# Kernel optimization log

Measured on AMD Instinct MI355X. Metric: run time of the kernel, lower is better.

Reference implementation:

```python
import jax, jax.numpy as jnp
import numpy as np

C = 128      # in = out channels
H = 4        # heads
HD = C // H  # head dim
N_DRUG, N_DIS, E = 50000, 20000, 250000
EA_DIM = 8


def _seg_softmax(logits, seg, n):
    # torch_geometric.utils.softmax: per-destination-node softmax over incident edges
    m = jax.ops.segment_max(logits, seg, num_segments=n)          # [n,H]
    ex = jnp.exp(logits - m[seg])
    s = jax.ops.segment_sum(ex, seg, num_segments=n)
    return ex / (s[seg] + 1e-16)


def _edge_conv(src_x, dst_x, si, di, Ws, bs, Wd, bd, attn, gate, n_dst):
    msg_src = src_x[si] @ Ws + bs           # [E,C] gather + linear
    msg_dst = dst_x[di] @ Wd + bd
    msg = msg_src + msg_dst
    if gate is not None:
        msg = msg * gate
    e = msg.shape[0]
    mh = msg.reshape(e, H, HD)
    sh = msg_src.reshape(e, H, HD)
    dh = msg_dst.reshape(e, H, HD)
    logits = (sh * dh).sum(-1) / jnp.sqrt(jnp.float32(HD)) + (mh * attn).sum(-1)  # [E,H]
    w = _seg_softmax(logits, di, n_dst)
    out = (mh * w[..., None]).reshape(e, C)
    return jax.ops.segment_sum(out, di, num_segments=n_dst)      # [n_dst,C]


def setup_inputs() -> dict:
    key = jax.random.key(0)
    ks = jax.random.split(key, 24)
    s = 1.0 / np.sqrt(C)
    d = {
        'x_drug': jax.random.normal(ks[0], (N_DRUG, C), jnp.float32),
        'x_disease': jax.random.normal(ks[1], (N_DIS, C), jnp.float32),
        'ea_treats': jax.random.normal(ks[2], (E, EA_DIM), jnp.float32),
        'si_t': jax.random.randint(ks[3], (E,), 0, N_DRUG),
        'di_t': jax.random.randint(ks[4], (E,), 0, N_DIS),
        'si_r': jax.random.randint(ks[5], (E,), 0, N_DIS),
        'di_r': jax.random.randint(ks[6], (E,), 0, N_DRUG),
        'Ws_t': jax.random.normal(ks[7], (C, C), jnp.float32) * s,
        'bs_t': jnp.zeros((C,), jnp.float32),
        'Wd_t': jax.random.normal(ks[8], (C, C), jnp.float32) * s,
        'bd_t': jnp.zeros((C,), jnp.float32),
        'attn_t': jax.random.normal(ks[9], (1, H, HD), jnp.float32) * 0.1,
        'Wg1': jax.random.normal(ks[10], (EA_DIM, C), jnp.float32) * (1.0 / np.sqrt(EA_DIM)),
        'bg1': jnp.zeros((C,), jnp.float32),
        'Wg2': jax.random.normal(ks[11], (C, C), jnp.float32) * s,
        'bg2': jnp.zeros((C,), jnp.float32),
        'Ws_r': jax.random.normal(ks[12], (C, C), jnp.float32) * s,
        'bs_r': jnp.zeros((C,), jnp.float32),
        'Wd_r': jax.random.normal(ks[13], (C, C), jnp.float32) * s,
        'bd_r': jnp.zeros((C,), jnp.float32),
        'attn_r': jax.random.normal(ks[14], (1, H, HD), jnp.float32) * 0.1,
        'Wo_drug': jax.random.normal(ks[15], (C, C), jnp.float32) * s,
        'bo_drug': jnp.zeros((C,), jnp.float32),
        'Wo_dis': jax.random.normal(ks[16], (C, C), jnp.float32) * s,
        'bo_dis': jnp.zeros((C,), jnp.float32),
    }
    return d


def reference(x_drug, x_disease, ea_treats, si_t, di_t, si_r, di_r,
              Ws_t, bs_t, Wd_t, bd_t, attn_t, Wg1, bg1, Wg2, bg2,
              Ws_r, bs_r, Wd_r, bd_r, attn_r,
              Wo_drug, bo_drug, Wo_dis, bo_dis):
    # edge gate for (drug, treats, disease): continuous edge attrs -> Linear-GELU-Linear-Sigmoid
    gate = jax.nn.sigmoid(jax.nn.gelu(ea_treats @ Wg1 + bg1, approximate=False) @ Wg2 + bg2)
    aggr_dis = _edge_conv(x_drug, x_disease, si_t, di_t, Ws_t, bs_t, Wd_t, bd_t, attn_t, gate, N_DIS)
    aggr_drug = _edge_conv(x_disease, x_drug, si_r, di_r, Ws_r, bs_r, Wd_r, bd_r, attn_r, None, N_DRUG)
    # single message per node type -> mean is identity; then per-node-type lin_out
    out_drug = aggr_drug @ Wo_drug + bo_drug
    out_dis = aggr_dis @ Wo_dis + bo_dis
    return out_drug, out_dis
```

## Files before the change

kernel.cpp:

```cpp
#include <hip/hip_runtime.h>
#include <hip/hip_bf16.h>
#include <math.h>

#define N_DRUG 50000
#define N_DIS  20000
#define NE     250000
#define NE_PAD 250048

#define NB0 79
#define NBT 275

typedef __bf16 bf16x8 __attribute__((ext_vector_type(8)));
typedef __bf16 bf16x4 __attribute__((ext_vector_type(4)));
typedef __bf16 bf16x2 __attribute__((ext_vector_type(2)));
typedef float  f32x4  __attribute__((ext_vector_type(4)));
typedef float  f32x2  __attribute__((ext_vector_type(2)));

__device__ __forceinline__ bf16x8 bz8() {
  bf16x8 v;
  #pragma unroll
  for (int j = 0; j < 8; ++j) v[j] = (__bf16)0.f;
  return v;
}

__device__ __forceinline__ float gelu_fast(float x) {
  float ax = fabsf(x);
  float t = fmaf(ax, 0.019527f, 3.43654e-4f);
  t = fmaf(ax, t, 0.1151945f);
  t = fmaf(ax, t, 0.1968564f);
  float p = fmaf(ax, t, 1.0f);
  float p2 = p * p;
  float p4 = p2 * p2;
  float r = __builtin_amdgcn_rcpf(p4);
  float sel = (x >= 0.f) ? (2.0f - r) : r;
  return 0.5f * x * sel;
}

__device__ __forceinline__ float sigmoid_fast(float v) {
  return __builtin_amdgcn_rcpf(1.0f + __expf(-v));
}

template <int N>
__device__ __forceinline__ float dpp_ror(float v) {
  int r = __builtin_amdgcn_update_dpp(0, __builtin_bit_cast(int, v),
                                      0x120 | N, 0xF, 0xF, false);
  return __builtin_bit_cast(float, r);
}

struct Seg {
  const void* A[4];
  const float* W[4];
  const float* bias[4];
  void* out[4];
  int M[4];
  int bstart[5];
};

template <int AIN_BF16, int OUT_BF16>
__global__ __launch_bounds__(256)
void gemm_seg(Seg d)
{
  __shared__ __bf16 Wt[128][136];

  const int b = blockIdx.x;
  const int sidx = (b >= d.bstart[3]) ? 3 : (b >= d.bstart[2]) ? 2
                 : (b >= d.bstart[1]) ? 1 : 0;
  const int nb = d.bstart[sidx + 1] - d.bstart[sidx];
  const int lb = b - d.bstart[sidx];
  const float* W = d.W[sidx];
  const float* bias = d.bias[sidx];
  const int M = d.M[sidx];
  const int ntiles = (M + 63) >> 6;
  const int tid = threadIdx.x;
  const int wv = tid >> 6, lane = tid & 63;
  const int m16 = lane & 15, quad = lane >> 4;

  for (int idx = tid; idx < 16384; idx += 256) {
    int k = idx >> 7, n = idx & 127;
    Wt[n][k] = (__bf16)W[idx];
  }
  __syncthreads();

  float bv[8];
  #pragma unroll
  for (int ct = 0; ct < 8; ++ct) bv[ct] = bias[ct * 16 + m16];

  auto load_afr = [&](int t, bf16x8* afr) {
    const int arow = (t << 6) + wv * 16 + m16;
    const bool ok = (t < ntiles) && (arow < M);
    if (AIN_BF16) {
      const __bf16* ap = (const __bf16*)d.A[sidx] + (long)arow * 128 + quad * 8;
      #pragma unroll
      for (int kt = 0; kt < 4; ++kt)
        afr[kt] = ok ? *(const bf16x8*)(ap + kt * 32) : bz8();
    } else {
      const float* ap = (const float*)d.A[sidx] + (long)arow * 128 + quad * 8;
      #pragma unroll
      for (int kt = 0; kt < 4; ++kt) {
        bf16x8 v = bz8();
        if (ok) {
          f32x4 lo = *(const f32x4*)(ap + kt * 32);
          f32x4 hi = *(const f32x4*)(ap + kt * 32 + 4);
          #pragma unroll
          for (int j = 0; j < 4; ++j) { v[j] = (__bf16)lo[j]; v[4 + j] = (__bf16)hi[j]; }
        }
        afr[kt] = v;
      }
    }
  };

  bf16x8 afr[4];
  if (lb < ntiles) load_afr(lb, afr);

  for (int t = lb; t < ntiles; t += nb) {
    bf16x8 nafr[4];
    load_afr(t + nb, nafr);

    f32x4 acc[8];
    #pragma unroll
    for (int ct = 0; ct < 8; ++ct) acc[ct] = (f32x4){0.f, 0.f, 0.f, 0.f};
    #pragma unroll
    for (int kt = 0; kt < 4; ++kt) {
      #pragma unroll
      for (int ct = 0; ct < 8; ++ct) {
        bf16x8 bfr = *(const bf16x8*)&Wt[ct * 16 + m16][kt * 32 + quad * 8];
        acc[ct] = __builtin_amdgcn_mfma_f32_16x16x32_bf16(afr[kt], bfr, acc[ct], 0, 0, 0);
      }
    }

    const int rb = (t << 6) + wv * 16 + quad * 4;
    #pragma unroll
    for (int ct = 0; ct < 8; ++ct) {
      const int col = ct * 16 + m16;
      #pragma unroll
      for (int rg = 0; rg < 4; ++rg) {
        int gr = rb + rg;
        if (gr < M) {
          float v = acc[ct][rg] + bv[ct];
          if (OUT_BF16) ((__bf16*)d.out[sidx])[(long)gr * 128 + col] = (__bf16)v;
          else          ((float*)d.out[sidx])[(long)gr * 128 + col] = v;
        }
      }
    }
    #pragma unroll
    for (int kt = 0; kt < 4; ++kt) afr[kt] = nafr[kt];
  }
}

__global__ __launch_bounds__(256)
void gate_kernel(const float* __restrict__ EA, const float* __restrict__ W2,
                 const float* __restrict__ Wg1, const float* __restrict__ bg1,
                 const float* __restrict__ bg2, const int* __restrict__ sorted_t,
                 __bf16* __restrict__ out)
{
  __shared__ __bf16 Wt[128][132];
  __shared__ __bf16 H[64][132];
  const int tid = threadIdx.x;
  const int wv = tid >> 6, lane = tid & 63;
  const int m16 = lane & 15, quad = lane >> 4;

  for (int idx = tid; idx < 16384; idx += 256) {
    int k = idx >> 7, n = idx & 127;
    Wt[n][k] = (__bf16)W2[idx];
  }
  __syncthreads();

  bf16x8 b1[8];
  #pragma unroll
  for (int ct = 0; ct < 8; ++ct) {
    bf16x8 v = bz8();
    if (quad == 0) {
      #pragma unroll
      for (int j = 0; j < 8; ++j) v[j] = (__bf16)Wg1[j * 128 + ct * 16 + m16];
    }
    b1[ct] = v;
  }
  float b1v[8], b2v[8];
  #pragma unroll
  for (int ct = 0; ct < 8; ++ct) {
    b1v[ct] = bg1[ct * 16 + m16];
    b2v[ct] = bg2[ct * 16 + m16];
  }

  const int ntiles = (NE + 63) >> 6;
  const int hr = wv * 16 + quad * 4;
  const int ar = wv * 16 + m16;

  for (int t = blockIdx.x; t < ntiles; t += gridDim.x) {
    const int p = (t << 6) + wv * 16 + m16;

    bf16x8 a1 = bz8();
    if (quad == 0 && p < NE) {
      int e = sorted_t[p];
      f32x4 e0 = *(const f32x4*)(EA + (long)e * 8);
      f32x4 e1 = *(const f32x4*)(EA + (long)e * 8 + 4);
      #pragma unroll
      for (int j = 0; j < 4; ++j) { a1[j] = (__bf16)e0[j]; a1[4 + j] = (__bf16)e1[j]; }
    }
    f32x4 h[8];
    #pragma unroll
    for (int ct = 0; ct < 8; ++ct)
      h[ct] = __builtin_amdgcn_mfma_f32_16x16x32_bf16(a1, b1[ct], (f32x4){0.f,0.f,0.f,0.f}, 0, 0, 0);

    #pragma unroll
    for (int ct = 0; ct < 8; ++ct) {
      const int col = ct * 16 + m16;
      #pragma unroll
      for (int rg = 0; rg < 4; ++rg)
        H[hr + rg][col] = (__bf16)gelu_fast(h[ct][rg] + b1v[ct]);
    }
    asm volatile("s_waitcnt lgkmcnt(0)" ::: "memory");

    bf16x8 afr[4];
    #pragma unroll
    for (int kt = 0; kt < 4; ++kt)
      afr[kt] = *(const bf16x8*)&H[ar][kt * 32 + quad * 8];
    asm volatile("" ::: "memory");

    f32x4 acc[8];
    #pragma unroll
    for (int ct = 0; ct < 8; ++ct) acc[ct] = (f32x4){0.f, 0.f, 0.f, 0.f};
    #pragma unroll
    for (int kt = 0; kt < 4; ++kt) {
      #pragma unroll
      for (int ct = 0; ct < 8; ++ct) {
        bf16x8 bfr = *(const bf16x8*)&Wt[ct * 16 + m16][kt * 32 + quad * 8];
        acc[ct] = __builtin_amdgcn_mfma_f32_16x16x32_bf16(afr[kt], bfr, acc[ct], 0, 0, 0);
      }
    }

    const long rowbase = (long)(t << 6) + hr;
    #pragma unroll
    for (int ct = 0; ct < 8; ++ct) {
      const int col = ct * 16 + m16;
      #pragma unroll
      for (int rg = 0; rg < 4; ++rg)
        out[(rowbase + rg) * 128 + col] = (__bf16)sigmoid_fast(acc[ct][rg] + b2v[ct]);
    }
  }
}

__global__ __launch_bounds__(256)
void histo2(const int* __restrict__ di_t, const int* __restrict__ di_r,
            int* __restrict__ cnt_dis, int* __restrict__ cnt_drug, int half) {
  int b = blockIdx.x;
  if (b < half) {
    int i = b * 256 + threadIdx.x;
    if (i < NE) atomicAdd(&cnt_dis[di_t[i]], 1);
  } else {
    int i = (b - half) * 256 + threadIdx.x;
    if (i < NE) atomicAdd(&cnt_drug[di_r[i]], 1);
  }
}

__global__ __launch_bounds__(256)
void scatter2(const int* __restrict__ di_t, const int* __restrict__ di_r,
              const int* __restrict__ si_t, const int* __restrict__ si_r,
              int* __restrict__ cur_dis, int* __restrict__ cur_drug,
              int* __restrict__ sorted_t, int* __restrict__ ssrc_t,
              int* __restrict__ ssrc_r, int half) {
  int b = blockIdx.x;
  if (b < half) {
    int i = b * 256 + threadIdx.x;
    if (i < NE) {
      int p = atomicAdd(&cur_dis[di_t[i]], 1);
      sorted_t[p] = i;
      ssrc_t[p] = si_t[i];
    }
  } else {
    int i = (b - half) * 256 + threadIdx.x;
    if (i < NE) {
      int p = atomicAdd(&cur_drug[di_r[i]], 1);
      ssrc_r[p] = si_r[i];
    }
  }
}

__device__ __forceinline__ void seg_geom(int b, int& base, int& n, int& lb) {
  if (b < NB0) { base = 0;     n = 20000; lb = b; }
  else         { base = 20000; n = 50000; lb = b - NB0; }
}

__global__ __launch_bounds__(256)
void scan_partial(const int* __restrict__ cnt, int* __restrict__ bsum) {
  __shared__ int sh[256];
  int b = blockIdx.x, t = threadIdx.x;
  int base, n, lb; seg_geom(b, base, n, lb);
  int i = lb * 256 + t;
  sh[t] = (i < n) ? cnt[base + i] : 0;
  __syncthreads();
  for (int d = 1; d < 256; d <<= 1) {
    int vv = (t >= d) ? sh[t - d] : 0;
    __syncthreads();
    sh[t] += vv;
    __syncthreads();
  }
  if (t == 255) bsum[b] = sh[255];
}

__global__ __launch_bounds__(256)
void scan_final2(const int* __restrict__ cnt, const int* __restrict__ bsum,
                 int* __restrict__ offs, int* __restrict__ cursor) {
  __shared__ int v[512];
  __shared__ int f[512];
  __shared__ int sh[256];
  const int b = blockIdx.x, t = threadIdx.x;

  for (int i = t; i < 512; i += 256) {
    v[i] = (i < NBT) ? bsum[i] : 0;
    f[i] = (i == 0 || i == NB0 || i >= NBT) ? 1 : 0;
  }
  __syncthreads();
  for (int d = 1; d < 512; d <<= 1) {
    const int i0 = t, i1 = t + 256;
    int vv0 = 0, ff0 = 1, vv1 = 0, ff1 = 1;
    if (i0 >= d) { vv0 = v[i0 - d]; ff0 = f[i0 - d]; }
    if (i1 >= d) { vv1 = v[i1 - d]; ff1 = f[i1 - d]; }
    __syncthreads();
    if (i0 >= d && !f[i0]) { v[i0] += vv0; f[i0] |= ff0; }
    if (i1 >= d && !f[i1]) { v[i1] += vv1; f[i1] |= ff1; }
    __syncthreads();
  }
  const int bexc_b = v[b] - bsum[b];

  int base, n, lb; seg_geom(b, base, n, lb);
  int i = lb * 256 + t;
  int own = (i < n) ? cnt[base + i] : 0;
  sh[t] = own;
  __syncthreads();
  for (int d = 1; d < 256; d <<= 1) {
    int vv = (t >= d) ? sh[t - d] : 0;
    __syncthreads();
    sh[t] += vv;
    __syncthreads();
  }
  int off = bexc_b + sh[t] - own;
  if (i < n) { offs[base + i] = off; cursor[base + i] = off; }
}

#define AGG_STEP(XC, GC, XT, GT, JJ)                                      \
  {                                                                       \
    if ((JJ) + 8 < m) {                                                   \
      _Pragma("unroll")                                                   \
      for (int u = 0; u < 4; ++u) {                                       \
        XT[u] = row_load(s2[u]);                                          \
        if (isDis) GT[u] = gate_load((JJ) + 8 + u);                       \
      }                                                                   \
    }                                                                     \
    if ((JJ) + 12 < m) {                                                  \
      _Pragma("unroll")                                                   \
      for (int u = 0; u < 4; ++u) s2[u] = sfetch((JJ) + 12 + u);          \
    }                                                                     \
    float part[4], mm0[4], mm1[4];                                        \
    _Pragma("unroll")                                                     \
    for (int u = 0; u < 4; ++u) {                                         \
      float xs0 = (float)XC[u][0], xs1 = (float)XC[u][1];                 \
      float m0 = xs0 + xd0, m1 = xs1 + xd1;                               \
      if (isDis) { m0 *= (float)GC[u][0]; m1 *= (float)GC[u][1]; }        \
      mm0[u] = m0; mm1[u] = m1;                                           \
      part[u] = xs0 * xdl0 + xs1 * xdl1 + m0 * at0 + m1 * at1;            \
    }                                                                     \
    _Pragma("unroll")                                                     \
    for (int u = 0; u < 4; ++u) part[u] += dpp_ror<1>(part[u]);           \
    _Pragma("unroll")                                                     \
    for (int u = 0; u < 4; ++u) part[u] += dpp_ror<2>(part[u]);           \
    _Pragma("unroll")                                                     \
    for (int u = 0; u < 4; ++u) part[u] += dpp_ror<4>(part[u]);           \
    _Pragma("unroll")                                                     \
    for (int u = 0; u < 4; ++u) part[u] += dpp_ror<8>(part[u]);           \
    _Pragma("unroll")                                                     \
    for (int u = 0; u < 4; ++u) {                                         \
      float ex = ((JJ) + u < m) ? __builtin_amdgcn_exp2f(part[u]) : 0.f;  \
      n0 += mm0[u] * ex;                                                  \
      n1 += mm1[u] * ex;                                                  \
      den += ex;                                                          \
    }                                                                     \
  }

__global__ __launch_bounds__(256)
void aggregate2(const __bf16* __restrict__ Xs_t, const __bf16* __restrict__ Xd_t,
                const __bf16* __restrict__ Xs_r, const __bf16* __restrict__ Xd_r,
                const int* __restrict__ ssrc_t, const int* __restrict__ ssrc_r,
                const int* __restrict__ offs, const int* __restrict__ cnt,
                const __bf16* __restrict__ gate_s,
                const float* __restrict__ attn_t, const float* __restrict__ attn_r,
                __bf16* __restrict__ aggr_dis, __bf16* __restrict__ aggr_drug)
{
  const int gw0 = (int)((blockIdx.x * 256 + threadIdx.x) >> 6);
  if (gw0 >= N_DIS + N_DRUG) return;
  const int gw = __builtin_amdgcn_readfirstlane(gw0);
  const int lane = threadIdx.x & 63;
  const int c = lane * 2;
  const bool isDis = gw < N_DIS;
  const int node = isDis ? gw : gw - N_DIS;
  const __bf16* __restrict__ Xs = isDis ? Xs_t : Xs_r;
  const __bf16* __restrict__ Xd = isDis ? Xd_t : Xd_r;
  const int* __restrict__ ssrc = isDis ? ssrc_t : ssrc_r;
  const float* __restrict__ attn = isDis ? attn_t : attn_r;
  __bf16* __restrict__ outp = isDis ? aggr_dis : aggr_drug;
  const int Ns = isDis ? N_DRUG : N_DIS;

  const int start = __builtin_amdgcn_readfirstlane(offs[gw]);
  const int m     = __builtin_amdgcn_readfirstlane(cnt[gw]);

  const float LOG2E = 1.4426950408889634f;
  f32x2 at = *(const f32x2*)(attn + c);
  bf16x2 xdb = *(const bf16x2*)(Xd + (size_t)node * 128 + c);
  const float xd0 = (float)xdb[0], xd1 = (float)xdb[1];
  const float xdl0 = xd0 * (0.17677669529663687f * LOG2E);
  const float xdl1 = xd1 * (0.17677669529663687f * LOG2E);
  const float at0 = at[0] * LOG2E, at1 = at[1] * LOG2E;

  auto sfetch = [&](int jn) -> int {
    int idx = start + jn;
    if (idx > NE - 1) idx = NE - 1;
    int s = __builtin_amdgcn_readfirstlane(ssrc[idx]);
    return ((unsigned)s < (unsigned)Ns) ? s : 0;
  };
  auto row_load = [&](int s) -> bf16x2 {
    return *(const bf16x2*)(Xs + (size_t)s * 128 + c);
  };
  auto gate_load = [&](int jn) -> bf16x2 {
    return *(const bf16x2*)(gate_s + (size_t)(start + jn) * 128 + c);
  };

  const bf16x2 z2 = {(__bf16)0.f, (__bf16)0.f};
  bf16x2 xa[4], ga[4], xb[4], gb[4], xc[4], gc[4];
  #pragma unroll
  for (int u = 0; u < 4; ++u) {
    xa[u] = z2; ga[u] = z2; xb[u] = z2; gb[u] = z2; xc[u] = z2; gc[u] = z2;
  }

  int s0[4], s1[4], s2[4];
  #pragma unroll
  for (int u = 0; u < 4; ++u) s0[u] = sfetch(u);
  #pragma unroll
  for (int u = 0; u < 4; ++u) s1[u] = sfetch(4 + u);
  #pragma unroll
  for (int u = 0; u < 4; ++u) s2[u] = sfetch(8 + u);

  #pragma unroll
  for (int u = 0; u < 4; ++u) {
    xa[u] = row_load(s0[u]);
    if (isDis) ga[u] = gate_load(u);
  }
  if (m > 4) {
    #pragma unroll
    for (int u = 0; u < 4; ++u) {
      xb[u] = row_load(s1[u]);
      if (isDis) gb[u] = gate_load(4 + u);
    }
  }

  float n0 = 0.f, n1 = 0.f, den = 0.f;

  int j = 0;
  while (j < m) {
    AGG_STEP(xa, ga, xc, gc, j); j += 4; if (j >= m) break;
    AGG_STEP(xb, gb, xa, ga, j); j += 4; if (j >= m) break;
    AGG_STEP(xc, gc, xb, gb, j); j += 4;
  }

  float r = __builtin_amdgcn_rcpf(den + 1e-16f);
  bf16x2 o;
  o[0] = (__bf16)(n0 * r);
  o[1] = (__bf16)(n1 * r);
  *(bf16x2*)(outp + (size_t)node * 128 + c) = o;
}

extern "C" void kernel_launch(void* const* d_in, const int* in_sizes, int n_in,
                              void* d_out, int out_size, void* d_ws, size_t ws_size,
                              hipStream_t stream)
{
  const float* x_drug  = (const float*)d_in[0];
  const float* x_dis   = (const float*)d_in[1];
  const float* ea      = (const float*)d_in[2];
  const int*   si_t    = (const int*)d_in[3];
  const int*   di_t    = (const int*)d_in[4];
  const int*   si_r    = (const int*)d_in[5];
  const int*   di_r    = (const int*)d_in[6];
  const float* Ws_t    = (const float*)d_in[7];
  const float* bs_t    = (const float*)d_in[8];
  const float* Wd_t    = (const float*)d_in[9];
  const float* bd_t    = (const float*)d_in[10];
  const float* attn_t  = (const float*)d_in[11];
  const float* Wg1     = (const float*)d_in[12];
  const float* bg1     = (const float*)d_in[13];
  const float* Wg2     = (const float*)d_in[14];
  const float* bg2     = (const float*)d_in[15];
  const float* Ws_r    = (const float*)d_in[16];
  const float* bs_r    = (const float*)d_in[17];
  const float* Wd_r    = (const float*)d_in[18];
  const float* bd_r    = (const float*)d_in[19];
  const float* attn_r  = (const float*)d_in[20];
  const float* Wo_drug = (const float*)d_in[21];
  const float* bo_drug = (const float*)d_in[22];
  const float* Wo_dis  = (const float*)d_in[23];
  const float* bo_dis  = (const float*)d_in[24];

  __bf16* wsb      = (__bf16*)d_ws;
  __bf16* Xs_t     = wsb;
  __bf16* Xd_t     = Xs_t + 6400000;
  __bf16* Xs_r     = Xd_t + 2560000;
  __bf16* Xd_r     = Xs_r + 2560000;
  __bf16* gate     = Xd_r + 6400000;
  int* cnt_dis    = (int*)(gate + (long)NE_PAD * 128);
  int* cnt_drug   = cnt_dis + 20000;
  int* offs_dis   = cnt_drug + 50000;
  int* offs_drug  = offs_dis + 20000;
  int* cur_dis    = offs_drug + 50000;
  int* cur_drug   = cur_dis + 20000;
  int* sorted_t   = cur_drug + 50000;
  int* ssrc_t     = sorted_t + 250000;
  int* ssrc_r     = ssrc_t + 250000;
  int* bsum       = ssrc_r + 250000;
  int* bexc       = bsum + 512;

  __bf16* aggr_dis  = Xd_t;
  __bf16* aggr_drug = Xd_r;

  float* out_drug = (float*)d_out;
  float* out_dis  = out_drug + (long)N_DRUG * 128;

  hipMemsetAsync(cnt_dis, 0, 70000 * sizeof(int), stream);

  const int eb = (NE + 255) / 256;

  histo2<<<2 * eb, 256, 0, stream>>>(di_t, di_r, cnt_dis, cnt_drug, eb);
  scan_partial<<<NBT, 256, 0, stream>>>(cnt_dis, bsum);
  scan_final2<<<NBT, 256, 0, stream>>>(cnt_dis, bsum, offs_dis, cur_dis);
  scatter2<<<2 * eb, 256, 0, stream>>>(di_t, di_r, si_t, si_r, cur_dis, cur_drug,
                                       sorted_t, ssrc_t, ssrc_r, eb);

  Seg nd;
  nd.A[0] = x_drug; nd.W[0] = Ws_t; nd.bias[0] = bs_t; nd.out[0] = Xs_t; nd.M[0] = N_DRUG;
  nd.A[1] = x_dis;  nd.W[1] = Wd_t; nd.bias[1] = bd_t; nd.out[1] = Xd_t; nd.M[1] = N_DIS;
  nd.A[2] = x_dis;  nd.W[2] = Ws_r; nd.bias[2] = bs_r; nd.out[2] = Xs_r; nd.M[2] = N_DIS;
  nd.A[3] = x_drug; nd.W[3] = Wd_r; nd.bias[3] = bd_r; nd.out[3] = Xd_r; nd.M[3] = N_DRUG;
  nd.bstart[0] = 0; nd.bstart[1] = 274; nd.bstart[2] = 384; nd.bstart[3] = 494; nd.bstart[4] = 768;
  gemm_seg<0, 1><<<768, 256, 0, stream>>>(nd);

  gate_kernel<<<768, 256, 0, stream>>>(ea, Wg2, Wg1, bg1, bg2, sorted_t, gate);

  aggregate2<<<(N_DIS + N_DRUG + 3) / 4, 256, 0, stream>>>(
      Xs_t, Xd_t, Xs_r, Xd_r, ssrc_t, ssrc_r, offs_dis, cnt_dis,
      gate, attn_t, attn_r, aggr_dis, aggr_drug);

  Seg od;
  od.A[0] = aggr_drug; od.W[0] = Wo_drug; od.bias[0] = bo_drug; od.out[0] = out_drug; od.M[0] = N_DRUG;
  od.A[1] = aggr_dis;  od.W[1] = Wo_dis;  od.bias[1] = bo_dis;  od.out[1] = out_dis;  od.M[1] = N_DIS;
  od.A[2] = od.A[1];   od.W[2] = od.W[1]; od.bias[2] = od.bias[1]; od.out[2] = od.out[1]; od.M[2] = N_DIS;
  od.A[3] = od.A[1];   od.W[3] = od.W[1]; od.bias[3] = od.bias[1]; od.out[3] = od.out[1]; od.M[3] = N_DIS;
  od.bstart[0] = 0; od.bstart[1] = 548; od.bstart[2] = 768; od.bstart[3] = 768; od.bstart[4] = 768;
  gemm_seg<1, 0><<<768, 256, 0, stream>>>(od);
}
```

Measured before the change: 318.3 us.

## Software-pipeline edge gate kernel with prefetched edge attributes across tiles

Restructures the gate MLP tile loop into a software pipeline. The sorted edge index is fetched two tiles ahead and the edge attributes one tile ahead, and the first-layer MFMA plus GELU for the next tile runs before the second-layer GEMM of the current tile. The goal is to hide the global gather latency and the LDS round-trip behind compute. The cost is more registers and a prologue, and the next tile's H writes reuse the shared buffer right after afr is read.

```diff
diff --git a/kernel.cpp b/kernel.cpp
--- a/kernel.cpp
+++ b/kernel.cpp
@@ -183,25 +183,49 @@
   }
 
   const int ntiles = (NE + 63) >> 6;
+  const int S = gridDim.x;
   const int hr = wv * 16 + quad * 4;
   const int ar = wv * 16 + m16;
-
-  for (int t = blockIdx.x; t < ntiles; t += gridDim.x) {
-    const int p = (t << 6) + wv * 16 + m16;
-
+  const int prow = wv * 16 + m16;
+
+  const f32x4 z4 = {0.f, 0.f, 0.f, 0.f};
+  f32x4 e0n = z4, e1n = z4;
+  int eidx2 = 0;
+
+  const int t0 = blockIdx.x;
+
+  auto pack_a1 = [&](const f32x4& lo, const f32x4& hi) -> bf16x8 {
+    bf16x8 v;
+    #pragma unroll
+    for (int j = 0; j < 4; ++j) { v[j] = (__bf16)lo[j]; v[4 + j] = (__bf16)hi[j]; }
+    return v;
+  };
+
+  {
     bf16x8 a1 = bz8();
-    if (quad == 0 && p < NE) {
-      int e = sorted_t[p];
-      f32x4 e0 = *(const f32x4*)(EA + (long)e * 8);
-      f32x4 e1 = *(const f32x4*)(EA + (long)e * 8 + 4);
-      #pragma unroll
-      for (int j = 0; j < 4; ++j) { a1[j] = (__bf16)e0[j]; a1[4 + j] = (__bf16)e1[j]; }
+    if (quad == 0) {
+      const int p0 = (t0 << 6) + prow;
+      if (p0 < NE) {
+        int e = sorted_t[p0];
+        f32x4 lo = *(const f32x4*)(EA + (long)e * 8);
+        f32x4 hi = *(const f32x4*)(EA + (long)e * 8 + 4);
+        a1 = pack_a1(lo, hi);
+      }
+      if (t0 + S < ntiles) {
+        const int p1 = ((t0 + S) << 6) + prow;
+        int e1i = (p1 < NE) ? sorted_t[p1] : 0;
+        e0n = *(const f32x4*)(EA + (long)e1i * 8);
+        e1n = *(const f32x4*)(EA + (long)e1i * 8 + 4);
+      }
+      if (t0 + 2 * S < ntiles) {
+        const int p2 = ((t0 + 2 * S) << 6) + prow;
+        if (p2 < NE) eidx2 = sorted_t[p2];
+      }
     }
     f32x4 h[8];
     #pragma unroll
     for (int ct = 0; ct < 8; ++ct)
-      h[ct] = __builtin_amdgcn_mfma_f32_16x16x32_bf16(a1, b1[ct], (f32x4){0.f,0.f,0.f,0.f}, 0, 0, 0);
-
+      h[ct] = __builtin_amdgcn_mfma_f32_16x16x32_bf16(a1, b1[ct], z4, 0, 0, 0);
     #pragma unroll
     for (int ct = 0; ct < 8; ++ct) {
       const int col = ct * 16 + m16;
@@ -209,17 +233,49 @@
       for (int rg = 0; rg < 4; ++rg)
         H[hr + rg][col] = (__bf16)gelu_fast(h[ct][rg] + b1v[ct]);
     }
+  }
+
+  for (int t = t0; t < ntiles; t += S) {
     asm volatile("s_waitcnt lgkmcnt(0)" ::: "memory");
-
     bf16x8 afr[4];
     #pragma unroll
     for (int kt = 0; kt < 4; ++kt)
       afr[kt] = *(const bf16x8*)&H[ar][kt * 32 + quad * 8];
-    asm volatile("" ::: "memory");
+
+    bf16x8 a1n = bz8();
+    {
+      const int p1 = ((t + S) << 6) + prow;
+      if (quad == 0 && (t + S) < ntiles && p1 < NE) a1n = pack_a1(e0n, e1n);
+    }
+    f32x4 h2[8];
+    #pragma unroll
+    for (int ct = 0; ct < 8; ++ct)
+      h2[ct] = __builtin_amdgcn_mfma_f32_16x16x32_bf16(a1n, b1[ct], z4, 0, 0, 0);
+
+    if (quad == 0) {
+      if (t + 2 * S < ntiles) {
+        e0n = *(const f32x4*)(EA + (long)eidx2 * 8);
+        e1n = *(const f32x4*)(EA + (long)eidx2 * 8 + 4);
+      }
+      if (t + 3 * S < ntiles) {
+        const int p3 = ((t + 3 * S) << 6) + prow;
+        if (p3 < NE) eidx2 = sorted_t[p3];
+      }
+    }
+
+    if (t + S < ntiles) {
+      #pragma unroll
+      for (int ct = 0; ct < 8; ++ct) {
+        const int col = ct * 16 + m16;
+        #pragma unroll
+        for (int rg = 0; rg < 4; ++rg)
+          H[hr + rg][col] = (__bf16)gelu_fast(h2[ct][rg] + b1v[ct]);
+      }
+    }
 
     f32x4 acc[8];
     #pragma unroll
-    for (int ct = 0; ct < 8; ++ct) acc[ct] = (f32x4){0.f, 0.f, 0.f, 0.f};
+    for (int ct = 0; ct < 8; ++ct) acc[ct] = z4;
     #pragma unroll
     for (int kt = 0; kt < 4; ++kt) {
       #pragma unroll
```

After: 325.8 us. +2.3%, slower.

## Fuse histogram, scan and scatter into one cooperative kernel with grid syncs

Applied to the files above, without the earlier changes.

Replaces the memset plus four separate sorting kernels (histogram, partial scan, final scan, scatter) with a single cooperative kernel launched with 1792 blocks that uses grid-wide syncs between phases. The aim is to remove per-launch overhead and inter-kernel gaps in the counting-sort preprocessing. It relies on cooperative launch support and on all 1792 blocks being co-resident, and grid.sync itself has a cost. The scatter now uses a grid-stride loop, so the ordering of atomics changes but results are equivalent.

```diff
diff --git a/kernel.cpp b/kernel.cpp
--- a/kernel.cpp
+++ b/kernel.cpp
@@ -1,6 +1,9 @@
 #include <hip/hip_runtime.h>
 #include <hip/hip_bf16.h>
+#include <hip/hip_cooperative_groups.h>
 #include <math.h>
+
+namespace cg = cooperative_groups;
 
 #define N_DRUG 50000
 #define N_DIS  20000
@@ -240,102 +243,97 @@
   }
 }
 
-__global__ __launch_bounds__(256)
-void histo2(const int* __restrict__ di_t, const int* __restrict__ di_r,
-            int* __restrict__ cnt_dis, int* __restrict__ cnt_drug, int half) {
-  int b = blockIdx.x;
-  if (b < half) {
-    int i = b * 256 + threadIdx.x;
-    if (i < NE) atomicAdd(&cnt_dis[di_t[i]], 1);
-  } else {
-    int i = (b - half) * 256 + threadIdx.x;
-    if (i < NE) atomicAdd(&cnt_drug[di_r[i]], 1);
-  }
-}
-
-__global__ __launch_bounds__(256)
-void scatter2(const int* __restrict__ di_t, const int* __restrict__ di_r,
-              const int* __restrict__ si_t, const int* __restrict__ si_r,
-              int* __restrict__ cur_dis, int* __restrict__ cur_drug,
-              int* __restrict__ sorted_t, int* __restrict__ ssrc_t,
-              int* __restrict__ ssrc_r, int half) {
-  int b = blockIdx.x;
-  if (b < half) {
-    int i = b * 256 + threadIdx.x;
-    if (i < NE) {
-      int p = atomicAdd(&cur_dis[di_t[i]], 1);
-      sorted_t[p] = i;
-      ssrc_t[p] = si_t[i];
-    }
-  } else {
-    int i = (b - half) * 256 + threadIdx.x;
-    if (i < NE) {
-      int p = atomicAdd(&cur_drug[di_r[i]], 1);
-      ssrc_r[p] = si_r[i];
-    }
-  }
-}
-
 __device__ __forceinline__ void seg_geom(int b, int& base, int& n, int& lb) {
   if (b < NB0) { base = 0;     n = 20000; lb = b; }
   else         { base = 20000; n = 50000; lb = b - NB0; }
 }
 
 __global__ __launch_bounds__(256)
-void scan_partial(const int* __restrict__ cnt, int* __restrict__ bsum) {
-  __shared__ int sh[256];
-  int b = blockIdx.x, t = threadIdx.x;
-  int base, n, lb; seg_geom(b, base, n, lb);
-  int i = lb * 256 + t;
-  sh[t] = (i < n) ? cnt[base + i] : 0;
-  __syncthreads();
-  for (int d = 1; d < 256; d <<= 1) {
-    int vv = (t >= d) ? sh[t - d] : 0;
-    __syncthreads();
-    sh[t] += vv;
-    __syncthreads();
-  }
-  if (t == 255) bsum[b] = sh[255];
-}
-
-__global__ __launch_bounds__(256)
-void scan_final2(const int* __restrict__ cnt, const int* __restrict__ bsum,
-                 int* __restrict__ offs, int* __restrict__ cursor) {
+void sort_all(const int* __restrict__ di_t, const int* __restrict__ di_r,
+              const int* __restrict__ si_t, const int* __restrict__ si_r,
+              int* __restrict__ cnt, int* __restrict__ sorted_t,
+              int* __restrict__ ssrc_t, int* __restrict__ ssrc_r,
+              int* __restrict__ bsum)
+{
+  cg::grid_group grid = cg::this_grid();
   __shared__ int v[512];
   __shared__ int f[512];
   __shared__ int sh[256];
-  const int b = blockIdx.x, t = threadIdx.x;
-
-  for (int i = t; i < 512; i += 256) {
-    v[i] = (i < NBT) ? bsum[i] : 0;
-    f[i] = (i == 0 || i == NB0 || i >= NBT) ? 1 : 0;
-  }
-  __syncthreads();
-  for (int d = 1; d < 512; d <<= 1) {
-    const int i0 = t, i1 = t + 256;
-    int vv0 = 0, ff0 = 1, vv1 = 0, ff1 = 1;
-    if (i0 >= d) { vv0 = v[i0 - d]; ff0 = f[i0 - d]; }
-    if (i1 >= d) { vv1 = v[i1 - d]; ff1 = f[i1 - d]; }
+
+  const int gsz = gridDim.x * 256;
+  const int tid0 = blockIdx.x * 256 + threadIdx.x;
+  int* cnt_dis  = cnt;
+  int* cnt_drug = cnt + 20000;
+  int* offs     = cnt + 70000;
+  int* cursor   = cnt + 140000;
+
+  for (int i = tid0; i < 70000; i += gsz) cnt[i] = 0;
+  grid.sync();
+
+  for (int i = tid0; i < NE; i += gsz) atomicAdd(&cnt_dis[di_t[i]], 1);
+  for (int i = tid0; i < NE; i += gsz) atomicAdd(&cnt_drug[di_r[i]], 1);
+  grid.sync();
+
+  if (blockIdx.x < NBT) {
+    const int b = blockIdx.x, t = threadIdx.x;
+    int base, n, lb; seg_geom(b, base, n, lb);
+    int i = lb * 256 + t;
+    sh[t] = (i < n) ? cnt[base + i] : 0;
     __syncthreads();
-    if (i0 >= d && !f[i0]) { v[i0] += vv0; f[i0] |= ff0; }
-    if (i1 >= d && !f[i1]) { v[i1] += vv1; f[i1] |= ff1; }
+    for (int d = 1; d < 256; d <<= 1) {
+      int vv = (t >= d) ? sh[t - d] : 0;
+      __syncthreads();
+      sh[t] += vv;
+      __syncthreads();
+    }
+    if (t == 255) bsum[b] = sh[255];
+  }
+  grid.sync();
+
+  if (blockIdx.x < NBT) {
+    const int b = blockIdx.x, t = threadIdx.x;
+    for (int i = t; i < 512; i += 256) {
+      v[i] = (i < NBT) ? bsum[i] : 0;
+      f[i] = (i == 0 || i == NB0 || i >= NBT) ? 1 : 0;
+    }
     __syncthreads();
-  }
-  const int bexc_b = v[b] - bsum[b];
-
-  int base, n, lb; seg_geom(b, base, n, lb);
-  int i = lb * 256 + t;
-  int own = (i < n) ? cnt[base + i] : 0;
-  sh[t] = own;
-  __syncthreads();
-  for (int d = 1; d < 256; d <<= 1) {
-    int vv = (t >= d) ? sh[t - d] : 0;
+    for (int d = 1; d < 512; d <<= 1) {
+      const int i0 = t, i1 = t + 256;
+      int vv0 = 0, ff0 = 1, vv1 = 0, ff1 = 1;
+      if (i0 >= d) { vv0 = v[i0 - d]; ff0 = f[i0 - d]; }
+      if (i1 >= d) { vv1 = v[i1 - d]; ff1 = f[i1 - d]; }
+      __syncthreads();
+      if (i0 >= d && !f[i0]) { v[i0] += vv0; f[i0] |= ff0; }
+      if (i1 >= d && !f[i1]) { v[i1] += vv1; f[i1] |= ff1; }
+      __syncthreads();
+    }
+    const int bexc_b = v[b] - bsum[b];
+
+    int base, n, lb; seg_geom(b, base, n, lb);
+    int i = lb * 256 + t;
+    int own = (i < n) ? cnt[base + i] : 0;
+    sh[t] = own;
     __syncthreads();
-    sh[t] += vv;
-    __syncthreads();
-  }
-  int off = bexc_b + sh[t] - own;
-  if (i < n) { offs[base + i] = off; cursor[base + i] = off; }
+    for (int d = 1; d < 256; d <<= 1) {
+      int vv = (t >= d) ? sh[t - d] : 0;
+      __syncthreads();
+      sh[t] += vv;
+      __syncthreads();
+    }
+    int off = bexc_b + sh[t] - own;
+    if (i < n) { offs[base + i] = off; cursor[base + i] = off; }
+  }
+  grid.sync();
+
+  for (int i = tid0; i < NE; i += gsz) {
+    int p = atomicAdd(&cursor[di_t[i]], 1);
+    sorted_t[p] = i;
+    ssrc_t[p] = si_t[i];
+  }
+  for (int i = tid0; i < NE; i += gsz) {
+    int p = atomicAdd(&cursor[20000 + di_r[i]], 1);
+    ssrc_r[p] = si_r[i];
+  }
 }
 
 #define AGG_STEP(XC, GC, XT, GT, JJ)                                      \
@@ -522,15 +520,15 @@
   float* out_drug = (float*)d_out;
   float* out_dis  = out_drug + (long)N_DRUG * 128;
 
-  hipMemsetAsync(cnt_dis, 0, 70000 * sizeof(int), stream);
-
-  const int eb = (NE + 255) / 256;
-
-  histo2<<<2 * eb, 256, 0, stream>>>(di_t, di_r, cnt_dis, cnt_drug, eb);
-  scan_partial<<<NBT, 256, 0, stream>>>(cnt_dis, bsum);
-  scan_final2<<<NBT, 256, 0, stream>>>(cnt_dis, bsum, offs_dis, cur_dis);
-  scatter2<<<2 * eb, 256, 0, stream>>>(di_t, di_r, si_t, si_r, cur_dis, cur_drug,
-                                       sorted_t, ssrc_t, ssrc_r, eb);
+  {
+    void* args[] = {
+      (void*)&di_t, (void*)&di_r, (void*)&si_t, (void*)&si_r,
+      (void*)&cnt_dis, (void*)&sorted_t, (void*)&ssrc_t, (void*)&ssrc_r,
+      (void*)&bsum
+    };
+    hipLaunchCooperativeKernel((void*)sort_all, dim3(1792), dim3(256),
+                               args, 0, stream);
+  }
 
   Seg nd;
   nd.A[0] = x_drug; nd.W[0] = Ws_t; nd.bias[0] = bs_t; nd.out[0] = Xs_t; nd.M[0] = N_DRUG;
```

Result: slower. 945.6 us (+197.0%).
